# Kernel tuning notes

Hardware: AMD Instinct MI355X
Metric: run time of the kernel (lower is better)

Reference implementation:

```python
import jax, jax.numpy as jnp
import numpy as np
from itertools import permutations as _permutations

N_ORB = 64
N_ALPHA = 5
N_BETA = 5
TEMP = 1.0
PERMS5 = jnp.asarray(np.array(list(_permutations(range(5))), dtype=np.int32))  # (120, 5)


def setup_inputs() -> dict:
    key = jax.random.key(0)
    ks = jax.random.split(key, 16)
    B = 8192
    s = 0.02
    inp = {
        "uniform_alpha": jax.random.uniform(ks[0], (B, N_ORB), dtype=jnp.float32),
        "uniform_beta": jax.random.uniform(ks[1], (B, N_ORB), dtype=jnp.float32),
        # learnable params
        "alpha_logits": jax.random.normal(ks[2], (N_ORB,), dtype=jnp.float32) * s,
        # alpha_to_beta: Linear(n_orb,128) -> SiLU -> Linear(128,64)
        "W1": jax.random.normal(ks[3], (N_ORB, 128), dtype=jnp.float32) * s,
        "b1": jnp.zeros((128,), jnp.float32),
        "W2": jax.random.normal(ks[4], (128, 64), dtype=jnp.float32) * s,
        "b2": jnp.zeros((64,), jnp.float32),
        # beta_conditioned_scorer: Linear(n_orb+64,256)->SiLU->Linear(256,256)->SiLU->Linear(256,n_orb)
        "V1": jax.random.normal(ks[5], (N_ORB + 64, 256), dtype=jnp.float32) * s,
        "c1": jnp.zeros((256,), jnp.float32),
        "V2": jax.random.normal(ks[6], (256, 256), dtype=jnp.float32) * s,
        "c2": jnp.zeros((256,), jnp.float32),
        "V3": jax.random.normal(ks[7], (256, N_ORB), dtype=jnp.float32) * s,
        "c3": jnp.zeros((N_ORB,), jnp.float32),
    }
    return inp


def _gumbel_topk(logits, uniform, k):
    """Straight-through Gumbel top-k mask. logits, uniform: (B, n)."""
    g = -jnp.log(-jnp.log(jnp.maximum(uniform, 1e-10)))
    perturbed = (logits + g) / TEMP
    _, top_idx = jax.lax.top_k(perturbed, k)                      # (B, k)
    B = logits.shape[0]
    one_hot = jnp.zeros_like(logits).at[jnp.arange(B)[:, None], top_idx].set(1.0)
    soft = jax.nn.softmax(perturbed, axis=-1)
    return one_hot - jax.lax.stop_gradient(soft) + soft


def _exact_pl_log_prob(logits, selection, k, perms):
    """log P(unordered top-k set) under Plackett-Luce, exact over k! orderings.

    logits: (B, n); selection: (B, n) soft/hard mask; perms: (P, k) static.
    """
    B, n = logits.shape
    P = perms.shape[0]
    _, sel_idx = jax.lax.top_k(selection, k)
    sel_idx = jnp.sort(sel_idx, axis=-1)                          # (B, k)
    perm_idx = sel_idx[:, perms]                                  # (B, P, k)
    lg = logits[:, None, :]                                       # (B, 1, n)
    remaining = jnp.ones((B, P, n), dtype=bool)
    lp = jnp.zeros((B, P), logits.dtype)
    bi = jnp.arange(B)[:, None]
    pi = jnp.arange(P)[None, :]
    for step in range(k):  # k is small and static (5)
        masked = jnp.where(remaining, lg, -jnp.inf)
        logp = jax.nn.log_softmax(masked, axis=-1)                # (B, P, n)
        idx = perm_idx[:, :, step]                                # (B, P)
        lp = lp + jnp.take_along_axis(logp, idx[..., None], axis=-1)[..., 0]
        remaining = remaining.at[bi, pi, idx].set(False)
    return jax.scipy.special.logsumexp(lp, axis=-1)              # (B,)


def reference(uniform_alpha, uniform_beta, alpha_logits, W1, b1, W2, b2,
              V1, c1, V2, c2, V3, c3):
    B = uniform_alpha.shape[0]
    a_logits = jnp.broadcast_to(alpha_logits[None, :], (B, N_ORB))
    alpha_config = _gumbel_topk(a_logits, uniform_alpha, N_ALPHA)

    # alpha_to_beta MLP
    h = jax.nn.silu(alpha_config @ W1 + b1)
    alpha_context = h @ W2 + b2                                   # (B, 64)

    beta_input = jnp.concatenate([jnp.zeros((B, N_ORB), a_logits.dtype), alpha_context], axis=-1)
    z = jax.nn.silu(beta_input @ V1 + c1)
    z = jax.nn.silu(z @ V2 + c2)
    beta_logits = z @ V3 + c3                                     # (B, n_orb)

    beta_config = _gumbel_topk(beta_logits, uniform_beta, N_BETA)
    configs = jnp.concatenate([alpha_config, beta_config], axis=-1)

    lp_a = _exact_pl_log_prob(a_logits, alpha_config, N_ALPHA, PERMS5)
    lp_b = _exact_pl_log_prob(beta_logits, beta_config, N_BETA, PERMS5)
    log_probs = lp_a + lp_b
    return configs, log_probs
```

## Files before the change

kernel.cpp:

```cpp
#include <hip/hip_runtime.h>
#include <math.h>

#define NTH 1024
#define KP 264
#define SPB 16
#define OFF_W2 0
#define OFF_V1 16384
#define OFF_V2 49152
#define OFF_V3 180224
#define WS_USHORTS 212992
#define MFMA16 __builtin_amdgcn_mfma_f32_16x16x32_bf16

typedef __attribute__((ext_vector_type(8))) short s16x8;
typedef __attribute__((ext_vector_type(8))) unsigned short u16x8;
typedef __attribute__((ext_vector_type(4))) float f32x4;

__device__ __forceinline__ float waveSum(float v) {
#pragma unroll
  for (int off = 32; off; off >>= 1) v += __shfl_xor(v, off, 64);
  return v;
}

__device__ __forceinline__ float waveMax(float v) {
#pragma unroll
  for (int off = 32; off; off >>= 1) v = fmaxf(v, __shfl_xor(v, off, 64));
  return v;
}

__device__ __forceinline__ float siluf(float x) { return x / (1.0f + __expf(-x)); }

__device__ __forceinline__ unsigned short bround(float x) {
  unsigned u = __float_as_uint(x);
  return (unsigned short)((u + 0x7FFFu + ((u >> 16) & 1u)) >> 16);
}

__device__ __forceinline__ void bsplit(float x, unsigned short& h, unsigned short& l) {
  unsigned u = __float_as_uint(x);
  unsigned hb = (u + 0x7FFFu + ((u >> 16) & 1u)) >> 16;
  float hf = __uint_as_float(hb << 16);
  float lf = x - hf;
  unsigned ul = __float_as_uint(lf);
  unsigned lb = (ul + 0x7FFFu + ((ul >> 16) & 1u)) >> 16;
  h = (unsigned short)hb; l = (unsigned short)lb;
}

__device__ __forceinline__ float permSumT(const float se0, const float se1,
                                          const float se2, const float se3,
                                          const float se4, float Z, int lane,
                                          const unsigned short* __restrict__ sPerm) {
  float psum = 0.0f;
#pragma unroll
  for (int pp = 0; pp < 2; ++pp) {
    int p = lane + pp * 64;
    if (p < 120) {
      unsigned code = sPerm[p];
      float c = 0.0f;
      float prod = Z;
#pragma unroll
      for (int j = 0; j < 4; ++j) {
        int dg = (code >> (3 * j)) & 7;
        float ev = (dg == 0) ? se0 : (dg == 1) ? se1 : (dg == 2) ? se2
                 : (dg == 3) ? se3 : se4;
        c += ev;
        prod *= (Z - c);
      }
      psum += __builtin_amdgcn_rcpf(prod);
    }
  }
  return psum;
}

__device__ __forceinline__ int extractMax(float& vv, float ev, float lv,
                                          int lane, float& seo, float& lvo) {
  float m = waveMax(vv);
  unsigned long long b = __ballot(vv == m);
  int j = __ffsll(b) - 1;
  seo = __uint_as_float(__builtin_amdgcn_readlane(__float_as_uint(ev), j));
  lvo = __uint_as_float(__builtin_amdgcn_readlane(__float_as_uint(lv), j));
  vv = (lane == j) ? -INFINITY : vv;
  return j;
}

__device__ __forceinline__ float selectPL5(float lv, float ev, float Z, float g,
                                           float* __restrict__ gout, int lane,
                                           const unsigned short* __restrict__ sPerm,
                                           int* __restrict__ jr ) {
  float vv = lv + g;
  unsigned long long sb = 0;
  float se0, se1, se2, se3, se4, l0, l1, l2, l3, l4;
  int j;
  j = extractMax(vv, ev, lv, lane, se0, l0); sb |= 1ull << j; if (jr) jr[0] = j;
  j = extractMax(vv, ev, lv, lane, se1, l1); sb |= 1ull << j; if (jr) jr[1] = j;
  j = extractMax(vv, ev, lv, lane, se2, l2); sb |= 1ull << j; if (jr) jr[2] = j;
  j = extractMax(vv, ev, lv, lane, se3, l3); sb |= 1ull << j; if (jr) jr[3] = j;
  j = extractMax(vv, ev, lv, lane, se4, l4); sb |= 1ull << j; if (jr) jr[4] = j;
  gout[lane] = (float)((sb >> lane) & 1ull);
  float sl = (((l0 + l1) + l2) + l3) + l4;
  float S = waveSum(permSumT(se0, se1, se2, se3, se4, Z, lane, sPerm));
  return sl + __logf(S);
}

__global__ __launch_bounds__(256)
void pcf_prep(const float* __restrict__ W2, const float* __restrict__ V1,
              const float* __restrict__ V2, const float* __restrict__ V3,
              unsigned short* __restrict__ ws)
{
  int tid = blockIdx.x * 256 + threadIdx.x;
  const float* src; int N, Ks, dstoff, r;
  if (tid < 1024)       { src = W2;            N = 64;  Ks = 4; dstoff = OFF_W2; r = tid; }
  else if (tid < 3072)  { src = V1 + 64 * 256; N = 256; Ks = 2; dstoff = OFF_V1; r = tid - 1024; }
  else if (tid < 11264) { src = V2;            N = 256; Ks = 8; dstoff = OFF_V2; r = tid - 3072; }
  else                  { src = V3;            N = 64;  Ks = 8; dstoff = OFF_V3; r = tid - 11264; }
  int lane = r & 63, ts = r >> 6;
  int ks = ts % Ks, ct = ts / Ks;
  int n = ct * 16 + (lane & 15);
  int k0 = ks * 32 + (lane >> 4) * 8;
  u16x8 hv, lv;
#pragma unroll
  for (int j = 0; j < 8; ++j) {
    float x = src[(size_t)(k0 + j) * N + n];
    unsigned short h, l;
    bsplit(x, h, l);
    hv[j] = h; lv[j] = l;
  }
  unsigned short* dst = ws + dstoff + (size_t)ts * 1024 + lane * 8;
  *(u16x8*)dst = hv;
  *(u16x8*)(dst + 512) = lv;
}

__global__ __launch_bounds__(NTH, 8)
void pcf_mfma(const float* __restrict__ ua, const float* __restrict__ ub,
              const float* __restrict__ alog, const float* __restrict__ W1,
              const float* __restrict__ b1, const float* __restrict__ b2,
              const float* __restrict__ c1, const float* __restrict__ c2,
              const float* __restrict__ c3,
              const unsigned short* __restrict__ wt, float* __restrict__ out)
{
  __shared__ unsigned short sAhi[16 * KP];
  __shared__ unsigned short sBhi[16 * KP];
  __shared__ float sBL[SPB * 64];
  __shared__ unsigned short sPerm[128];

  const int t    = threadIdx.x;
  const int lane = t & 63;
  const int wv   = t >> 6;
  const int ln15 = lane & 15;
  const int quad = lane >> 4;
  const int bbase = blockIdx.x * SPB;

  if (t < 120) {
    int rem = t;
    unsigned avail = 0x43210u, code = 0;
#pragma unroll
    for (int j = 0; j < 4; ++j) {
      const int fct = (j == 0) ? 24 : (j == 1) ? 6 : (j == 2) ? 2 : 1;
      int q = rem / fct; rem -= q * fct;
      int sh = q * 4;
      unsigned dg = (avail >> sh) & 0xF;
      avail = (avail & ((1u << sh) - 1u)) | ((avail >> (sh + 4)) << sh);
      code |= dg << (3 * j);
    }
    sPerm[t] = (unsigned short)code;
  }

  float gb, uA;
  {
    int b = bbase + wv;
    float u = ub[(size_t)b * 64 + lane];
    gb = -logf(-logf(fmaxf(u, 1e-10f)));
    uA = ua[(size_t)b * 64 + lane];
  }
  __syncthreads();

  float lpA;
  {
    float la = alog[lane];
    float ea = __expf(la);
    float Za = waveSum(ea);
    int b = bbase + wv;
    float ga = -logf(-logf(fmaxf(uA, 1e-10f)));
    int jr[5];
    lpA = selectPL5(la, ea, Za, ga, out + (size_t)b * 128, lane, sPerm, jr);

    int jcol = lane * 2;
    float2 a = *(const float2*)(b1 + jcol);
#pragma unroll
    for (int r = 0; r < 5; ++r) {
      float2 w = *(const float2*)(W1 + (size_t)jr[r] * 128 + jcol);
      a.x += w.x; a.y += w.y;
    }
    unsigned h0 = bround(siluf(a.x));
    unsigned h1 = bround(siluf(a.y));
    *(unsigned*)&sAhi[wv * KP + jcol] = h0 | (h1 << 16);
  }
  __syncthreads();

  if (wv < 4) {
    f32x4 acc = {0.f, 0.f, 0.f, 0.f};
#pragma unroll
    for (int ks = 0; ks < 4; ++ks) {
      int ko = ks * 32 + quad * 8;
      s16x8 ah = *(const s16x8*)&sAhi[ln15 * KP + ko];
      const unsigned short* tsb = wt + OFF_W2 + (size_t)(wv * 4 + ks) * 1024;
      s16x8 bh = ((const s16x8*)tsb)[lane];
      s16x8 bl = ((const s16x8*)(tsb + 512))[lane];
      acc = MFMA16(ah, bh, acc, 0, 0, 0);
      acc = MFMA16(ah, bl, acc, 0, 0, 0);
    }
    int col = wv * 16 + ln15;
    float bias = b2[col];
#pragma unroll
    for (int r = 0; r < 4; ++r)
      sBhi[(quad * 4 + r) * KP + col] = bround(acc[r] + bias);
  }
  __syncthreads();

  {
    f32x4 acc = {0.f, 0.f, 0.f, 0.f};
#pragma unroll
    for (int ks = 0; ks < 2; ++ks) {
      int ko = ks * 32 + quad * 8;
      s16x8 ah = *(const s16x8*)&sBhi[ln15 * KP + ko];
      const unsigned short* tsb = wt + OFF_V1 + (size_t)(wv * 2 + ks) * 1024;
      s16x8 bh = ((const s16x8*)tsb)[lane];
      s16x8 bl = ((const s16x8*)(tsb + 512))[lane];
      acc = MFMA16(ah, bh, acc, 0, 0, 0);
      acc = MFMA16(ah, bl, acc, 0, 0, 0);
    }
    int col = wv * 16 + ln15;
    float bias = c1[col];
#pragma unroll
    for (int r = 0; r < 4; ++r)
      sAhi[(quad * 4 + r) * KP + col] = bround(siluf(acc[r] + bias));
  }
  __syncthreads();

  {
    f32x4 acc = {0.f, 0.f, 0.f, 0.f};
#pragma unroll 4
    for (int ks = 0; ks < 8; ++ks) {
      int ko = ks * 32 + quad * 8;
      s16x8 ah = *(const s16x8*)&sAhi[ln15 * KP + ko];
      const unsigned short* tsb = wt + OFF_V2 + (size_t)(wv * 8 + ks) * 1024;
      s16x8 bh = ((const s16x8*)tsb)[lane];
      s16x8 bl = ((const s16x8*)(tsb + 512))[lane];
      acc = MFMA16(ah, bh, acc, 0, 0, 0);
      acc = MFMA16(ah, bl, acc, 0, 0, 0);
    }
    int col = wv * 16 + ln15;
    float bias = c2[col];
#pragma unroll
    for (int r = 0; r < 4; ++r)
      sBhi[(quad * 4 + r) * KP + col] = bround(siluf(acc[r] + bias));
  }
  __syncthreads();

  if (wv < 4) {
    f32x4 acc = {0.f, 0.f, 0.f, 0.f};
#pragma unroll
    for (int ks = 0; ks < 8; ++ks) {
      int ko = ks * 32 + quad * 8;
      s16x8 ah = *(const s16x8*)&sBhi[ln15 * KP + ko];
      const unsigned short* tsb = wt + OFF_V3 + (size_t)(wv * 8 + ks) * 1024;
      s16x8 bh = ((const s16x8*)tsb)[lane];
      s16x8 bl = ((const s16x8*)(tsb + 512))[lane];
      acc = MFMA16(ah, bh, acc, 0, 0, 0);
      acc = MFMA16(ah, bl, acc, 0, 0, 0);
    }
    int col = wv * 16 + ln15;
    float bias = c3[col];
#pragma unroll
    for (int r = 0; r < 4; ++r)
      sBL[(quad * 4 + r) * 64 + col] = acc[r] + bias;
  }
  __syncthreads();

  {
    int b = bbase + wv;
    float blv = sBL[wv * 64 + lane];
    float eb = __expf(blv);
    float Zb = waveSum(eb);
    float lp = selectPL5(blv, eb, Zb, gb, out + (size_t)b * 128 + 64, lane,
                         sPerm, nullptr);
    if (lane == 0)
      out[(size_t)8192 * 128 + b] = lpA + lp;
  }
}

__device__ __forceinline__ float permSum(const float se0, const float se1,
                                         const float se2, const float se3,
                                         const float se4, float Z, int lane) {
  float psum = 0.0f;
#pragma unroll
  for (int pp = 0; pp < 2; ++pp) {
    int p = lane + pp * 64;
    if (p < 120) {
      int rem = p;
      unsigned avail = 0x43210u;
      float c = 0.0f;
      float prod = Z;
#pragma unroll
      for (int j = 0; j < 4; ++j) {
        const int fct = (j == 0) ? 24 : (j == 1) ? 6 : (j == 2) ? 2 : 1;
        int q = rem / fct; rem -= q * fct;
        int sh = q * 4;
        int dg = (avail >> sh) & 0xF;
        avail = (avail & ((1u << sh) - 1u)) | ((avail >> (sh + 4)) << sh);
        float ev = (dg == 0) ? se0 : (dg == 1) ? se1 : (dg == 2) ? se2
                 : (dg == 3) ? se3 : se4;
        c += ev;
        prod *= (Z - c);
      }
      psum += __builtin_amdgcn_rcpf(prod);
    }
  }
  return psum;
}

__device__ __forceinline__ float selectAndPL(float lv, float ev, float Z,
                                             float g,
                                             float* __restrict__ gout,
                                             int lane,
                                             float* __restrict__ sValsRow,
                                             float* __restrict__ sSelERow,
                                             int* __restrict__ selIdxRow) {
  float v = lv + g;
  sValsRow[lane] = v;
  int rank = 0;
#pragma unroll
  for (int j = 0; j < 16; ++j) {
    float4 w = *(const float4*)&sValsRow[j * 4];
    int base = j * 4;
    rank += (w.x > v || (w.x == v && base + 0 < lane)) ? 1 : 0;
    rank += (w.y > v || (w.y == v && base + 1 < lane)) ? 1 : 0;
    rank += (w.z > v || (w.z == v && base + 2 < lane)) ? 1 : 0;
    rank += (w.w > v || (w.w == v && base + 3 < lane)) ? 1 : 0;
  }
  bool sel = rank < 5;
  gout[lane] = sel ? 1.0f : 0.0f;
  if (sel) {
    sSelERow[rank] = ev;
    sSelERow[8 + rank] = lv;
    if (selIdxRow) selIdxRow[rank] = lane;
  }
  float se0 = sSelERow[0], se1 = sSelERow[1], se2 = sSelERow[2],
        se3 = sSelERow[3], se4 = sSelERow[4];
  float sl = sSelERow[8] + sSelERow[9] + sSelERow[10] + sSelERow[11]
           + sSelERow[12];
  float S = waveSum(permSum(se0, se1, se2, se3, se4, Z, lane));
  return sl + __logf(S);
}

#define SPB4 4
__global__ __launch_bounds__(256, 8)
void pcf_small(const float* __restrict__ ua, const float* __restrict__ ub,
               const float* __restrict__ alog, const float* __restrict__ W1,
               const float* __restrict__ b1, const float* __restrict__ W2,
               const float* __restrict__ b2, const float* __restrict__ V1,
               const float* __restrict__ c1, const float* __restrict__ V2,
               const float* __restrict__ c2, const float* __restrict__ V3,
               const float* __restrict__ c3, float* __restrict__ out)
{
  __shared__ float sA[SPB4 * 256];
  __shared__ float sB[SPB4 * 256];
  __shared__ float sP[4 * 256];
  __shared__ float sVals[4 * 64];
  __shared__ float sSelE[4 * 16];
  __shared__ int   sSelA[SPB4 * 5];
  __shared__ float sLpA[SPB4];

  const int t    = threadIdx.x;
  const int lane = t & 63;
  const int wv   = t >> 6;
  const int bbase = blockIdx.x * SPB4;

  float* sValsRow = &sVals[wv * 64];
  float* sSelERow = &sSelE[wv * 16];

  {
    float la = alog[lane];
    float ea = __expf(la);
    float Za = waveSum(ea);
    int b = bbase + wv;
    float u = ua[(size_t)b * 64 + lane];
    float g = -logf(-logf(fmaxf(u, 1e-10f)));
    float lp = selectAndPL(la, ea, Za, g, out + (size_t)b * 128, lane,
                           sValsRow, sSelERow, &sSelA[wv * 5]);
    if (lane == 0) sLpA[wv] = lp;
  }
  __syncthreads();
  {
    int s = wv;
    int i0 = sSelA[s * 5 + 0], i1 = sSelA[s * 5 + 1], i2 = sSelA[s * 5 + 2];
    int i3 = sSelA[s * 5 + 3], i4 = sSelA[s * 5 + 4];
#pragma unroll
    for (int jh = 0; jh < 2; ++jh) {
      int j = lane + jh * 64;
      float acc = b1[j] + W1[i0 * 128 + j] + W1[i1 * 128 + j]
                + W1[i2 * 128 + j] + W1[i3 * 128 + j] + W1[i4 * 128 + j];
      sA[s * 128 + j] = siluf(acc);
    }
  }
  __syncthreads();
  {
    float acc[SPB4] = {};
    const int kb = 32 * wv;
#pragma unroll 2
    for (int m = 0; m < 8; ++m) {
      int k0 = kb + 4 * m;
      float w0 = W2[(k0 + 0) * 64 + lane];
      float w1 = W2[(k0 + 1) * 64 + lane];
      float w2 = W2[(k0 + 2) * 64 + lane];
      float w3 = W2[(k0 + 3) * 64 + lane];
#pragma unroll
      for (int s = 0; s < SPB4; ++s) {
        float4 x = *(float4*)&sA[s * 128 + k0];
        acc[s] += x.x * w0 + x.y * w1 + x.z * w2 + x.w * w3;
      }
    }
#pragma unroll
    for (int s = 0; s < SPB4; ++s) sP[wv * 256 + s * 64 + lane] = acc[s];
  }
  __syncthreads();
  {
    int o = t;
    float v = b2[o & 63] + sP[o] + sP[256 + o] + sP[512 + o] + sP[768 + o];
    sB[o] = v;
  }
  __syncthreads();
  {
    const int c = 64 * wv + lane;
    float acc[SPB4];
    float cb = c1[c];
#pragma unroll
    for (int s = 0; s < SPB4; ++s) acc[s] = cb;
    const float* wp = V1 + (size_t)64 * 256 + c;
#pragma unroll 4
    for (int m = 0; m < 16; ++m) {
      int k0 = 4 * m;
      float w0 = wp[(k0 + 0) * 256];
      float w1 = wp[(k0 + 1) * 256];
      float w2 = wp[(k0 + 2) * 256];
      float w3 = wp[(k0 + 3) * 256];
#pragma unroll
      for (int s = 0; s < SPB4; ++s) {
        float4 x = *(float4*)&sB[s * 64 + k0];
        acc[s] += x.x * w0 + x.y * w1 + x.z * w2 + x.w * w3;
      }
    }
#pragma unroll
    for (int s = 0; s < SPB4; ++s) sA[s * 256 + c] = siluf(acc[s]);
  }
  __syncthreads();
  {
    const int c = 64 * wv + lane;
    float acc[SPB4];
    float cb = c2[c];
#pragma unroll
    for (int s = 0; s < SPB4; ++s) acc[s] = cb;
    const float* wp = V2 + c;
#pragma unroll 4
    for (int m = 0; m < 64; ++m) {
      int k0 = 4 * m;
      float w0 = wp[(size_t)(k0 + 0) * 256];
      float w1 = wp[(size_t)(k0 + 1) * 256];
      float w2 = wp[(size_t)(k0 + 2) * 256];
      float w3 = wp[(size_t)(k0 + 3) * 256];
#pragma unroll
      for (int s = 0; s < SPB4; ++s) {
        float4 x = *(float4*)&sA[s * 256 + k0];
        acc[s] += x.x * w0 + x.y * w1 + x.z * w2 + x.w * w3;
      }
    }
#pragma unroll
    for (int s = 0; s < SPB4; ++s) sB[s * 256 + c] = siluf(acc[s]);
  }
  __syncthreads();
  {
    float acc[SPB4] = {};
    const int kb = 64 * wv;
#pragma unroll 4
    for (int m = 0; m < 16; ++m) {
      int k0 = kb + 4 * m;
      float w0 = V3[(k0 + 0) * 64 + lane];
      float w1 = V3[(k0 + 1) * 64 + lane];
      float w2 = V3[(k0 + 2) * 64 + lane];
      float w3 = V3[(k0 + 3) * 64 + lane];
#pragma unroll
      for (int s = 0; s < SPB4; ++s) {
        float4 x = *(float4*)&sB[s * 256 + k0];
        acc[s] += x.x * w0 + x.y * w1 + x.z * w2 + x.w * w3;
      }
    }
#pragma unroll
    for (int s = 0; s < SPB4; ++s) sP[wv * 256 + s * 64 + lane] = acc[s];
  }
  __syncthreads();
  {
    int b = bbase + wv;
    float blv = c3[lane] + sP[wv * 64 + lane] + sP[256 + wv * 64 + lane]
              + sP[512 + wv * 64 + lane] + sP[768 + wv * 64 + lane];
    float eb = __expf(blv);
    float Zb = waveSum(eb);
    float u = ub[(size_t)b * 64 + lane];
    float g = -logf(-logf(fmaxf(u, 1e-10f)));
    float lp = selectAndPL(blv, eb, Zb, g, out + (size_t)b * 128 + 64, lane,
                           sValsRow, sSelERow, nullptr);
    if (lane == 0)
      out[(size_t)8192 * 128 + b] = sLpA[wv] + lp;
  }
}

extern "C" void kernel_launch(void* const* d_in, const int* in_sizes, int n_in,
                              void* d_out, int out_size, void* d_ws, size_t ws_size,
                              hipStream_t stream) {
  const float* ua   = (const float*)d_in[0];
  const float* ub   = (const float*)d_in[1];
  const float* alog = (const float*)d_in[2];
  const float* W1   = (const float*)d_in[3];
  const float* b1   = (const float*)d_in[4];
  const float* W2   = (const float*)d_in[5];
  const float* b2   = (const float*)d_in[6];
  const float* V1   = (const float*)d_in[7];
  const float* c1   = (const float*)d_in[8];
  const float* V2   = (const float*)d_in[9];
  const float* c2   = (const float*)d_in[10];
  const float* V3   = (const float*)d_in[11];
  const float* c3   = (const float*)d_in[12];
  float* out = (float*)d_out;

  if (ws_size >= (size_t)WS_USHORTS * 2) {
    unsigned short* wt = (unsigned short*)d_ws;
    pcf_prep<<<dim3(52), dim3(256), 0, stream>>>(W2, V1, V2, V3, wt);
    pcf_mfma<<<dim3(8192 / SPB), dim3(NTH), 0, stream>>>(
        ua, ub, alog, W1, b1, b2, c1, c2, c3, wt, out);
  } else {
    pcf_small<<<dim3(8192 / SPB4), dim3(256), 0, stream>>>(
        ua, ub, alog, W1, b1, W2, b2, V1, c1, V2, c2, V3, c3, out);
  }
}
```

Baseline: 99.63 us.

## Halve block to 8 waves, each handling two samples and two column tiles

Shrinks the block from 16 to 8 wavefronts while keeping 16 samples per block. Each wave now runs the selection and Plackett-Luce work for two samples, and computes two 16-column output tiles in the 256-wide layers. The aim is to reuse the A-fragment loaded from LDS across two MFMAs, cut per-block sync overhead, and allow more blocks to be resident. The cost is more serial work per wave and higher register pressure; the sequential selectPL5 calls also lengthen the critical path.

```diff
diff --git a/kernel.cpp b/kernel.cpp
--- a/kernel.cpp
+++ b/kernel.cpp
@@ -1,7 +1,7 @@
 #include <hip/hip_runtime.h>
 #include <math.h>
 
-#define NTH 1024
+#define NTH 512
 #define KP 264
 #define SPB 16
 #define OFF_W2 0
@@ -147,6 +147,8 @@
   const int ln15 = lane & 15;
   const int quad = lane >> 4;
   const int bbase = blockIdx.x * SPB;
+  const int s0 = 2 * wv, s1 = 2 * wv + 1;
+  const int bI0 = bbase + s0, bI1 = bbase + s1;
 
   if (t < 120) {
     int rem = t;
@@ -163,35 +165,53 @@
     sPerm[t] = (unsigned short)code;
   }
 
-  float gb, uA;
-  {
-    int b = bbase + wv;
-    float u = ub[(size_t)b * 64 + lane];
-    gb = -logf(-logf(fmaxf(u, 1e-10f)));
-    uA = ua[(size_t)b * 64 + lane];
-  }
-  __syncthreads();
-
-  float lpA;
+  float gb0, gb1, uA0, uA1;
+  {
+    float u0 = ub[(size_t)bI0 * 64 + lane];
+    float u1 = ub[(size_t)bI1 * 64 + lane];
+    gb0 = -logf(-logf(fmaxf(u0, 1e-10f)));
+    gb1 = -logf(-logf(fmaxf(u1, 1e-10f)));
+    uA0 = ua[(size_t)bI0 * 64 + lane];
+    uA1 = ua[(size_t)bI1 * 64 + lane];
+  }
+  __syncthreads();
+
+  float lpA0, lpA1;
   {
     float la = alog[lane];
     float ea = __expf(la);
     float Za = waveSum(ea);
-    int b = bbase + wv;
-    float ga = -logf(-logf(fmaxf(uA, 1e-10f)));
-    int jr[5];
-    lpA = selectPL5(la, ea, Za, ga, out + (size_t)b * 128, lane, sPerm, jr);
-
-    int jcol = lane * 2;
-    float2 a = *(const float2*)(b1 + jcol);
-#pragma unroll
-    for (int r = 0; r < 5; ++r) {
-      float2 w = *(const float2*)(W1 + (size_t)jr[r] * 128 + jcol);
-      a.x += w.x; a.y += w.y;
-    }
-    unsigned h0 = bround(siluf(a.x));
-    unsigned h1 = bround(siluf(a.y));
-    *(unsigned*)&sAhi[wv * KP + jcol] = h0 | (h1 << 16);
+    const int jcol = lane * 2;
+    float2 bias1 = *(const float2*)(b1 + jcol);
+
+    {
+      float ga = -logf(-logf(fmaxf(uA0, 1e-10f)));
+      int jr[5];
+      lpA0 = selectPL5(la, ea, Za, ga, out + (size_t)bI0 * 128, lane, sPerm, jr);
+      float2 a = bias1;
+#pragma unroll
+      for (int r = 0; r < 5; ++r) {
+        float2 w = *(const float2*)(W1 + (size_t)jr[r] * 128 + jcol);
+        a.x += w.x; a.y += w.y;
+      }
+      unsigned h0 = bround(siluf(a.x));
+      unsigned h1 = bround(siluf(a.y));
+      *(unsigned*)&sAhi[s0 * KP + jcol] = h0 | (h1 << 16);
+    }
+    {
+      float ga = -logf(-logf(fmaxf(uA1, 1e-10f)));
+      int jr[5];
+      lpA1 = selectPL5(la, ea, Za, ga, out + (size_t)bI1 * 128, lane, sPerm, jr);
+      float2 a = bias1;
+#pragma unroll
+      for (int r = 0; r < 5; ++r) {
+        float2 w = *(const float2*)(W1 + (size_t)jr[r] * 128 + jcol);
+        a.x += w.x; a.y += w.y;
+      }
+      unsigned h0 = bround(siluf(a.x));
+      unsigned h1 = bround(siluf(a.y));
+      *(unsigned*)&sAhi[s1 * KP + jcol] = h0 | (h1 << 16);
+    }
   }
   __syncthreads();
 
@@ -216,42 +236,60 @@
   __syncthreads();
 
   {
-    f32x4 acc = {0.f, 0.f, 0.f, 0.f};
+    const int ct0 = wv, ct1 = wv + 8;
+    f32x4 acc0 = {0.f, 0.f, 0.f, 0.f};
+    f32x4 acc1 = {0.f, 0.f, 0.f, 0.f};
 #pragma unroll
     for (int ks = 0; ks < 2; ++ks) {
       int ko = ks * 32 + quad * 8;
       s16x8 ah = *(const s16x8*)&sBhi[ln15 * KP + ko];
-      const unsigned short* tsb = wt + OFF_V1 + (size_t)(wv * 2 + ks) * 1024;
-      s16x8 bh = ((const s16x8*)tsb)[lane];
-      s16x8 bl = ((const s16x8*)(tsb + 512))[lane];
-      acc = MFMA16(ah, bh, acc, 0, 0, 0);
-      acc = MFMA16(ah, bl, acc, 0, 0, 0);
-    }
-    int col = wv * 16 + ln15;
-    float bias = c1[col];
-#pragma unroll
-    for (int r = 0; r < 4; ++r)
-      sAhi[(quad * 4 + r) * KP + col] = bround(siluf(acc[r] + bias));
-  }
-  __syncthreads();
-
-  {
-    f32x4 acc = {0.f, 0.f, 0.f, 0.f};
-#pragma unroll 4
+      const unsigned short* tb0 = wt + OFF_V1 + (size_t)(ct0 * 2 + ks) * 1024;
+      const unsigned short* tb1 = wt + OFF_V1 + (size_t)(ct1 * 2 + ks) * 1024;
+      s16x8 b0h = ((const s16x8*)tb0)[lane];
+      s16x8 b0l = ((const s16x8*)(tb0 + 512))[lane];
+      s16x8 b1h = ((const s16x8*)tb1)[lane];
+      s16x8 b1l = ((const s16x8*)(tb1 + 512))[lane];
+      acc0 = MFMA16(ah, b0h, acc0, 0, 0, 0);
+      acc0 = MFMA16(ah, b0l, acc0, 0, 0, 0);
+      acc1 = MFMA16(ah, b1h, acc1, 0, 0, 0);
+      acc1 = MFMA16(ah, b1l, acc1, 0, 0, 0);
+    }
+    int col0 = ct0 * 16 + ln15, col1 = ct1 * 16 + ln15;
+    float bias0 = c1[col0], bias1v = c1[col1];
+#pragma unroll
+    for (int r = 0; r < 4; ++r) {
+      sAhi[(quad * 4 + r) * KP + col0] = bround(siluf(acc0[r] + bias0));
+      sAhi[(quad * 4 + r) * KP + col1] = bround(siluf(acc1[r] + bias1v));
+    }
+  }
+  __syncthreads();
+
+  {
+    const int ct0 = wv, ct1 = wv + 8;
+    f32x4 acc0 = {0.f, 0.f, 0.f, 0.f};
+    f32x4 acc1 = {0.f, 0.f, 0.f, 0.f};
+#pragma unroll 2
     for (int ks = 0; ks < 8; ++ks) {
       int ko = ks * 32 + quad * 8;
       s16x8 ah = *(const s16x8*)&sAhi[ln15 * KP + ko];
-      const unsigned short* tsb = wt + OFF_V2 + (size_t)(wv * 8 + ks) * 1024;
-      s16x8 bh = ((const s16x8*)tsb)[lane];
-      s16x8 bl = ((const s16x8*)(tsb + 512))[lane];
-      acc = MFMA16(ah, bh, acc, 0, 0, 0);
-      acc = MFMA16(ah, bl, acc, 0, 0, 0);
-    }
-    int col = wv * 16 + ln15;
-    float bias = c2[col];
-#pragma unroll
-    for (int r = 0; r < 4; ++r)
-      sBhi[(quad * 4 + r) * KP + col] = bround(siluf(acc[r] + bias));
+      const unsigned short* tb0 = wt + OFF_V2 + (size_t)(ct0 * 8 + ks) * 1024;
+      const unsigned short* tb1 = wt + OFF_V2 + (size_t)(ct1 * 8 + ks) * 1024;
+      s16x8 b0h = ((const s16x8*)tb0)[lane];
+      s16x8 b0l = ((const s16x8*)(tb0 + 512))[lane];
+      s16x8 b1h = ((const s16x8*)tb1)[lane];
+      s16x8 b1l = ((const s16x8*)(tb1 + 512))[lane];
+      acc0 = MFMA16(ah, b0h, acc0, 0, 0, 0);
+      acc0 = MFMA16(ah, b0l, acc0, 0, 0, 0);
+      acc1 = MFMA16(ah, b1h, acc1, 0, 0, 0);
+      acc1 = MFMA16(ah, b1l, acc1, 0, 0, 0);
+    }
+    int col0 = ct0 * 16 + ln15, col1 = ct1 * 16 + ln15;
+    float bias0 = c2[col0], bias1v = c2[col1];
+#pragma unroll
+    for (int r = 0; r < 4; ++r) {
+      sBhi[(quad * 4 + r) * KP + col0] = bround(siluf(acc0[r] + bias0));
+      sBhi[(quad * 4 + r) * KP + col1] = bround(siluf(acc1[r] + bias1v));
+    }
   }
   __syncthreads();
 
@@ -276,14 +314,20 @@
   __syncthreads();
 
   {
-    int b = bbase + wv;
-    float blv = sBL[wv * 64 + lane];
-    float eb = __expf(blv);
-    float Zb = waveSum(eb);
-    float lp = selectPL5(blv, eb, Zb, gb, out + (size_t)b * 128 + 64, lane,
-                         sPerm, nullptr);
-    if (lane == 0)
-      out[(size_t)8192 * 128 + b] = lpA + lp;
+    float blv0 = sBL[s0 * 64 + lane];
+    float eb0 = __expf(blv0);
+    float Zb0 = waveSum(eb0);
+    float lp0 = selectPL5(blv0, eb0, Zb0, gb0, out + (size_t)bI0 * 128 + 64,
+                          lane, sPerm, nullptr);
+    float blv1 = sBL[s1 * 64 + lane];
+    float eb1 = __expf(blv1);
+    float Zb1 = waveSum(eb1);
+    float lp1 = selectPL5(blv1, eb1, Zb1, gb1, out + (size_t)bI1 * 128 + 64,
+                          lane, sPerm, nullptr);
+    if (lane == 0) {
+      out[(size_t)8192 * 128 + bI0] = lpA0 + lp0;
+      out[(size_t)8192 * 128 + bI1] = lpA1 + lp1;
+    }
   }
 }
 
```

Measured after the change: 107.1 us. 7.5% more time.
